# Optimization experiments

Measured on AMD Instinct MI355X. Metric: run time of the kernel, lower is better.

The kernel has to match this reference:

```python
import jax, jax.numpy as jnp
import numpy as np
import math

EMB = 2048
NH = 16
HD = EMB // NH
T = 4096
EPS = 1e-5


def setup_inputs() -> dict:
    key = jax.random.key(0)
    ks = jax.random.split(key, 8)
    lim = 1.0 / math.sqrt(EMB)
    q = jax.random.normal(ks[0], (T, EMB), dtype=jnp.float32)
    k = jax.random.normal(ks[1], (T, EMB), dtype=jnp.float32)
    v = jax.random.normal(ks[2], (T, EMB), dtype=jnp.float32)
    Wq = jax.random.uniform(ks[3], (EMB, EMB), minval=-lim, maxval=lim, dtype=jnp.float32)
    Wk = jax.random.uniform(ks[4], (EMB, EMB), minval=-lim, maxval=lim, dtype=jnp.float32)
    Wv = jax.random.uniform(ks[5], (EMB, EMB), minval=-lim, maxval=lim, dtype=jnp.float32)
    Wo = jax.random.uniform(ks[6], (EMB, EMB), minval=-lim, maxval=lim, dtype=jnp.float32)
    ln_w = jnp.ones((EMB,), dtype=jnp.float32)
    mask = jnp.tril(jnp.ones((T, T), dtype=jnp.int32))  # causal
    return {"q": q, "k": k, "v": v, "Wq": Wq, "Wk": Wk, "Wv": Wv,
            "Wo": Wo, "ln_w": ln_w, "mask": mask}


def reference(q, k, v, Wq, Wk, Wv, Wo, ln_w, mask):
    scale = 1.0 / math.sqrt(HD)
    # projections (Linear is weight @ x, i.e. x @ W^T)
    Q = (q @ Wq.T).reshape(T, NH, HD).transpose(1, 0, 2)   # [nh, T, hd]
    K = (k @ Wk.T).reshape(T, NH, HD).transpose(1, 0, 2)
    V = (v @ Wv.T).reshape(T, NH, HD).transpose(1, 0, 2)
    A = jnp.einsum('htd,hsd->hts', Q, K) * scale           # [nh, T, T]
    A = jnp.where(mask != 0, A, -jnp.inf)
    P = jax.nn.softmax(A, axis=-1)
    y = jnp.einsum('hts,hsd->htd', P, V)                   # [nh, T, hd]
    y = y.transpose(1, 0, 2).reshape(T, EMB)               # concat heads
    y = y @ Wo.T
    # deterministic dropout = identity; add residue; per-token LayerNorm (scale only)
    x = y + q
    mu = jnp.mean(x, axis=-1, keepdims=True)
    var = jnp.var(x, axis=-1, keepdims=True)
    return (x - mu) * jax.lax.rsqrt(var + EPS) * ln_w
```

## Files before the change

### kernel.cpp

```cpp
#include <hip/hip_runtime.h>

typedef __bf16 bf16x8 __attribute__((ext_vector_type(8)));
typedef __bf16 bf16x2_t __attribute__((ext_vector_type(2)));
typedef float f32x4 __attribute__((ext_vector_type(4)));
typedef float f32x16 __attribute__((ext_vector_type(16)));
typedef unsigned int u32x4 __attribute__((ext_vector_type(4)));
typedef unsigned short u16x8 __attribute__((ext_vector_type(8)));

#define EMB 2048
#define NH 16
#define HD 128
#define TSEQ 4096

__device__ __forceinline__ unsigned short f2bf(float x) {
  unsigned int u = __builtin_bit_cast(unsigned int, x);
  u += 0x7fffu + ((u >> 16) & 1u);
  return (unsigned short)(u >> 16);
}

__device__ __forceinline__ float bf2f(unsigned short u) {
  unsigned int x = ((unsigned int)u) << 16;
  return __builtin_bit_cast(float, x);
}

__device__ __forceinline__ float ex2(float x) { return __builtin_amdgcn_exp2f(x); }

__device__ __forceinline__ void gl_lds16(const void* g, void* l) {
  __builtin_amdgcn_global_load_lds((__attribute__((address_space(1))) void*)(void*)g,
                                   (__attribute__((address_space(3))) void*)l, 16, 0, 0);
}

template <typename OutT>
__device__ __forceinline__ void store_out(OutT* p, float v) {
  if constexpr (sizeof(OutT) == 2) { *p = f2bf(v); } else { *p = v; }
}

__global__ __launch_bounds__(256) void cvt_all(const float* __restrict__ q, const float* __restrict__ k,
                                               const float* __restrict__ v, const float* __restrict__ Wq,
                                               const float* __restrict__ Wk, const float* __restrict__ Wv,
                                               const float* __restrict__ Wo,
                                               unsigned short* qb, unsigned short* kb, unsigned short* vb,
                                               unsigned short* Wqb, unsigned short* Wkb, unsigned short* Wvb,
                                               unsigned short* Wob) {
  const int SX = TSEQ * EMB / 8;
  const int SW = EMB * EMB / 8;
  int i = blockIdx.x * 256 + threadIdx.x;
  const float* src; unsigned short* dst; int off;
  if (i < 3 * SX) {
    int seg = i >> 20; off = i & (SX - 1);
    src = (seg == 0) ? q : (seg == 1) ? k : v;
    dst = (seg == 0) ? qb : (seg == 1) ? kb : vb;
  } else {
    int j = i - 3 * SX;
    int seg = j >> 19; off = j & (SW - 1);
    src = (seg == 0) ? Wq : (seg == 1) ? Wk : (seg == 2) ? Wv : Wo;
    dst = (seg == 0) ? Wqb : (seg == 1) ? Wkb : (seg == 2) ? Wvb : Wob;
  }
  const float4* p = (const float4*)src + (size_t)off * 2;
  float4 a = p[0], b = p[1];
  u32x4 r;
  r.x = (unsigned)f2bf(a.x) | ((unsigned)f2bf(a.y) << 16);
  r.y = (unsigned)f2bf(a.z) | ((unsigned)f2bf(a.w) << 16);
  r.z = (unsigned)f2bf(b.x) | ((unsigned)f2bf(b.y) << 16);
  r.w = (unsigned)f2bf(b.z) | ((unsigned)f2bf(b.w) << 16);
  ((u32x4*)dst)[off] = r;
}

template <typename OutT>
__device__ __forceinline__ void gemm_body(const unsigned short* __restrict__ A,
                                          const unsigned short* __restrict__ B,
                                          OutT* __restrict__ C,
                                          int m0, int n0, int N, int K, char* smem, float oscale) {
  const int t = threadIdx.x;
  const int l = t & 63, lg = l >> 4, l15 = l & 15;
  const int w = t >> 6, wm = w >> 1, wn = w & 1;

  f32x4 acc[4][4] = {};

  const int rowS = t >> 2;
  const int cbS = (t & 3) * 16;
  const int swS = cbS ^ ((rowS & 3) << 4);
  const char* Ab = (const char*)A + ((size_t)(m0 + rowS) * K) * 2;
  const char* Bb = (const char*)B + ((size_t)(n0 + rowS) * K) * 2;
  const size_t rowStep = (size_t)64 * K * 2;

  auto stage = [&](int buf, int kt) {
    const int ktB = kt * 2;
    char* sA = smem + buf * 8192;
    char* sB = smem + 16384 + buf * 8192;
    gl_lds16(Ab + ktB + swS, sA + t * 16);
    gl_lds16(Ab + rowStep + ktB + swS, sA + 4096 + t * 16);
    gl_lds16(Bb + ktB + swS, sB + t * 16);
    gl_lds16(Bb + rowStep + ktB + swS, sB + 4096 + t * 16);
  };

  const int nIter = K / 32;
  stage(0, 0);
  int cur = 0;
  for (int it = 0; it < nIter; ++it) {
    if (it + 1 < nIter) {
      stage(cur ^ 1, (it + 1) * 32);
      asm volatile("s_waitcnt vmcnt(4)" ::: "memory");
    } else {
      asm volatile("s_waitcnt vmcnt(0)" ::: "memory");
    }
    __builtin_amdgcn_s_barrier();

    const char* sA = smem + cur * 8192;
    const char* sB = smem + 16384 + cur * 8192;
    const int rsw = (l15 & 3) << 4;
    bf16x8 af[4], bfr[4];
#pragma unroll
    for (int m = 0; m < 4; m++) {
      const int r = wm * 64 + m * 16 + l15;
      af[m] = *(const bf16x8*)(sA + r * 64 + ((lg * 16) ^ rsw));
    }
#pragma unroll
    for (int n = 0; n < 4; n++) {
      const int r = wn * 64 + n * 16 + l15;
      bfr[n] = *(const bf16x8*)(sB + r * 64 + ((lg * 16) ^ rsw));
    }
#pragma unroll
    for (int m = 0; m < 4; m++)
#pragma unroll
      for (int n = 0; n < 4; n++)
        acc[m][n] = __builtin_amdgcn_mfma_f32_16x16x32_bf16(af[m], bfr[n], acc[m][n], 0, 0, 0);

    __builtin_amdgcn_s_barrier();
    cur ^= 1;
  }

#pragma unroll
  for (int m = 0; m < 4; m++) {
    int row = m0 + wm * 64 + m * 16 + 4 * lg;
#pragma unroll
    for (int n = 0; n < 4; n++) {
      int col = n0 + wn * 64 + n * 16 + l15;
#pragma unroll
      for (int i = 0; i < 4; i++)
        store_out(C + (size_t)(row + i) * N + col, acc[m][n][i] * oscale);
    }
  }
}

__global__ __launch_bounds__(256) void gemm_qkv(const unsigned short* __restrict__ qb,
                                                const unsigned short* __restrict__ kb,
                                                const unsigned short* __restrict__ vb,
                                                const unsigned short* __restrict__ Wq,
                                                const unsigned short* __restrict__ Wk,
                                                const unsigned short* __restrict__ Wv,
                                                unsigned short* Qo, unsigned short* Ko, unsigned short* Vto) {
  __shared__ char smem[32768];
  const int bx = blockIdx.x;
  const int z = bx >> 9, r = bx & 511;
  const unsigned short* A; const unsigned short* B; unsigned short* C;
  int N, m0, n0; float sc;
  if (z == 0)      { A = qb; B = Wq; C = Qo;  N = EMB;  n0 = (r & 15) << 7; m0 = (r >> 4) << 7; sc = 0.12751743f; }
  else if (z == 1) { A = kb; B = Wk; C = Ko;  N = EMB;  n0 = (r & 15) << 7; m0 = (r >> 4) << 7; sc = 1.0f; }
  else             { A = Wv; B = vb; C = Vto; N = TSEQ; n0 = (r & 31) << 7; m0 = (r >> 5) << 7; sc = 1.0f; }
  gemm_body<unsigned short>(A, B, C, m0, n0, N, EMB, smem, sc);
}

__global__ __launch_bounds__(256) void gemm_o(const unsigned short* __restrict__ A,
                                              const unsigned short* __restrict__ B,
                                              float* __restrict__ C) {
  __shared__ char smem[32768];
  gemm_body<float>(A, B, C, blockIdx.y * 128, blockIdx.x * 128, EMB, EMB, smem, 1.0f);
}

__global__ __launch_bounds__(256, 2) void attn_kernel(const unsigned short* __restrict__ Q,
                                                      const unsigned short* __restrict__ Kp,
                                                      const unsigned short* __restrict__ Vt,
                                                      unsigned short* __restrict__ slots,
                                                      float* __restrict__ lbuf) {
  __shared__ char sK[2][16384];
  __shared__ char sV[3][16384];
  const int t = threadIdx.x, l = t & 63, w = t >> 6;
  const int l31 = l & 31, hh = l >> 5;
  const int b = blockIdx.x;
  const int h = b >> 5;
  const int p = (b >> 1) & 15;
  const int half = b & 1;
  const int slotBase = (h * 16 + p) * 3;

  const int q0A = 128 * p, q0B = 128 * (31 - p);
  const int swi = (half == 0) ? (2 * p + 2) : 64;
  const int kvOff = 31 - 2 * p;

  int q0 = (half == 0) ? q0A : q0B;
  int qrow = q0 + w * 32 + l31;

  auto kvof = [&](int gi) -> int {
    if (half == 0) return (gi < swi) ? gi * 64 : (gi - swi) * 64;
    return (kvOff + gi) * 64;
  };

  bf16x8 qf[8];
#pragma unroll
  for (int kd = 0; kd < 8; kd++)
    qf[kd] = *(const bf16x8*)(Q + (size_t)qrow * EMB + h * HD + kd * 16 + hh * 8);

  f32x16 o[4] = {};
  float l_run = 0.0f;

  const int rK = t >> 4, cK = (t & 15) * 16;
  const int rV = t >> 3, cV = (t & 7) * 16;
  const char* Kb = (const char*)Kp;
  const char* Vb = (const char*)Vt;

  auto stage = [&](int kbuf, int vbuf, int kv0) {
#pragma unroll
    for (int c = 0; c < 4; c++) {
      int rowK = c * 16 + rK;
      gl_lds16(Kb + (size_t)(kv0 + rowK) * (EMB * 2) + h * (HD * 2) + (cK ^ ((rowK & 15) << 4)),
               sK[kbuf] + c * 4096 + t * 16);
      int rowV = c * 32 + rV;
      gl_lds16(Vb + (size_t)(h * HD + rowV) * (TSEQ * 2) + kv0 * 2 + (cV ^ ((rowV & 7) << 4)),
               sV[vbuf] + c * 4096 + t * 16);
    }
  };

  auto writeout = [&](int slotId) {
    unsigned short* S = slots + (size_t)slotId * (128 * 128);
    const int r = w * 32 + l31;
    float lt = l_run + __shfl_xor(l_run, 32, 64);
    if (hh == 0) lbuf[slotId * 128 + r] = lt;
#pragma unroll
    for (int hdm = 0; hdm < 4; hdm++)
#pragma unroll
      for (int rq = 0; rq < 4; rq++) {
        ushort4 st;
        st.x = f2bf(o[hdm][4 * rq + 0]);
        st.y = f2bf(o[hdm][4 * rq + 1]);
        st.z = f2bf(o[hdm][4 * rq + 2]);
        st.w = f2bf(o[hdm][4 * rq + 3]);
        *(ushort4*)(S + r * 128 + hdm * 32 + 8 * rq + 4 * hh) = st;
      }
  };

  stage(0, 0, kvof(0));
  int kc = 0, vc = 0, vn = 1;
  for (int gi = 0; gi < 33; ++gi) {
    if (half == 0 && gi == swi) {
      writeout(slotBase + 0);
#pragma unroll
      for (int hdm = 0; hdm < 4; hdm++)
#pragma unroll
        for (int i = 0; i < 16; i++) o[hdm][i] = 0.0f;
      l_run = 0.0f;
      q0 = q0B;
      qrow = q0 + w * 32 + l31;
#pragma unroll
      for (int kd = 0; kd < 8; kd++)
        qf[kd] = *(const bf16x8*)(Q + (size_t)qrow * EMB + h * HD + kd * 16 + hh * 8);
    }
    const int kv0 = kvof(gi);
    if (gi + 1 < 33) {
      stage(kc ^ 1, vn, kvof(gi + 1));
      asm volatile("s_waitcnt vmcnt(8)" ::: "memory");
    } else {
      asm volatile("s_waitcnt vmcnt(0)" ::: "memory");
    }
    __builtin_amdgcn_s_barrier();

    const char* KB = sK[kc];
    const char* VB = sV[vc];

    f32x16 s[2];
#pragma unroll
    for (int i = 0; i < 16; i++) { s[0][i] = -8.0f; s[1][i] = -8.0f; }
    __builtin_amdgcn_s_setprio(1);
#pragma unroll
    for (int kvm = 0; kvm < 2; kvm++) {
      const int rowA = kvm * 32 + l31;
      const int swz = (rowA & 15) << 4;
#pragma unroll
      for (int kd = 0; kd < 8; kd++) {
        bf16x8 kf = *(const bf16x8*)(KB + rowA * 256 + ((kd * 32 + hh * 16) ^ swz));
        s[kvm] = __builtin_amdgcn_mfma_f32_32x32x16_bf16(kf, qf[kd], s[kvm], 0, 0, 0);
      }
    }
    __builtin_amdgcn_s_setprio(0);
    __builtin_amdgcn_s_barrier();

    const bool diag = (kv0 + 64 > q0);
    if (diag) {
#pragma unroll
      for (int kvm = 0; kvm < 2; kvm++)
#pragma unroll
        for (int i = 0; i < 16; i++)
          if (kv0 + kvm * 32 + (i & 3) + 8 * (i >> 2) + 4 * hh > qrow) s[kvm][i] = -1e30f;
    }
    float psum = 0.0f;
    unsigned int wb[16];
#pragma unroll
    for (int kvm = 0; kvm < 2; kvm++)
#pragma unroll
      for (int m = 0; m < 8; m++) {
        float p0 = ex2(s[kvm][2 * m + 0]);
        float p1 = ex2(s[kvm][2 * m + 1]);
        psum += p0 + p1;
        bf16x2_t pk; pk[0] = (__bf16)p0; pk[1] = (__bf16)p1;
        wb[kvm * 8 + m] = __builtin_bit_cast(unsigned int, pk);
      }
    l_run += psum;

    __builtin_amdgcn_s_setprio(1);
#pragma unroll
    for (int kvm = 0; kvm < 2; kvm++)
#pragma unroll
      for (int sx = 0; sx < 2; sx++) {
        const int base = kvm * 8 + 4 * sx;
        const unsigned int a0 = wb[base + 0], a1 = wb[base + 1];
        const unsigned int b0 = wb[base + 2], b1 = wb[base + 3];
        const unsigned int snd0 = hh ? a0 : b0;
        const unsigned int snd1 = hh ? a1 : b1;
        const unsigned int rcv0 = (unsigned int)__shfl_xor((int)snd0, 32, 64);
        const unsigned int rcv1 = (unsigned int)__shfl_xor((int)snd1, 32, 64);
        u32x4 pw;
        pw.x = hh ? rcv0 : a0;
        pw.y = hh ? rcv1 : a1;
        pw.z = hh ? b0 : rcv0;
        pw.w = hh ? b1 : rcv1;
        const bf16x8 pfrag = __builtin_bit_cast(bf16x8, pw);
        const int ks = kvm * 2 + sx;
#pragma unroll
        for (int hdm = 0; hdm < 4; hdm++) {
          const int rowA = hdm * 32 + l31;
          bf16x8 vf = *(const bf16x8*)(VB + rowA * 128 + ((ks * 32 + hh * 16) ^ ((rowA & 7) << 4)));
          o[hdm] = __builtin_amdgcn_mfma_f32_32x32x16_bf16(vf, pfrag, o[hdm], 0, 0, 0);
        }
      }
    __builtin_amdgcn_s_setprio(0);

    kc ^= 1;
    vc = vn;
    vn = (vn == 2) ? 0 : vn + 1;
  }

  writeout(slotBase + ((half == 0) ? 1 : 2));
}

__global__ __launch_bounds__(256) void merge_kernel(const unsigned short* __restrict__ slots,
                                                    const float* __restrict__ lbuf,
                                                    unsigned short* __restrict__ Y) {
  const int tile = blockIdx.x;
  const int h = tile >> 5, tt = tile & 31;
  const int p = (tt <= 15) ? tt : 31 - tt;
  const int base = (h * 16 + p) * 3;
  const int t = threadIdx.x;
  const int r = t >> 1;
  const int c0 = (t & 1) * 64;
  unsigned short* yp = Y + (size_t)(128 * tt + r) * EMB + h * HD + c0;
  if (tt <= 15) {
    const unsigned short* S = slots + (size_t)(base + 0) * (128 * 128) + r * 128 + c0;
    const float inv = 1.0f / lbuf[(base + 0) * 128 + r];
#pragma unroll
    for (int j = 0; j < 8; j++) {
      u16x8 a = ((const u16x8*)S)[j];
      u16x8 ov;
#pragma unroll
      for (int e = 0; e < 8; e++) ov[e] = f2bf(bf2f(a[e]) * inv);
      ((u16x8*)yp)[j] = ov;
    }
  } else {
    const unsigned short* S0 = slots + (size_t)(base + 1) * (128 * 128) + r * 128 + c0;
    const unsigned short* S1 = slots + (size_t)(base + 2) * (128 * 128) + r * 128 + c0;
    const float inv = 1.0f / (lbuf[(base + 1) * 128 + r] + lbuf[(base + 2) * 128 + r]);
#pragma unroll
    for (int j = 0; j < 8; j++) {
      u16x8 a = ((const u16x8*)S0)[j];
      u16x8 c = ((const u16x8*)S1)[j];
      u16x8 ov;
#pragma unroll
      for (int e = 0; e < 8; e++) ov[e] = f2bf((bf2f(a[e]) + bf2f(c[e])) * inv);
      ((u16x8*)yp)[j] = ov;
    }
  }
}

__global__ __launch_bounds__(256) void ln_kernel(const float* __restrict__ y2,
                                                 const float* __restrict__ qin,
                                                 const float* __restrict__ lnw,
                                                 float* __restrict__ out) {
  const int row = blockIdx.x, t = threadIdx.x;
  const float4* Y = (const float4*)(y2 + (size_t)row * EMB);
  const float4* Qv = (const float4*)(qin + (size_t)row * EMB);
  float4 a = Y[t], b = Qv[t];
  float4 x0, x1;
  x0.x = a.x + b.x; x0.y = a.y + b.y; x0.z = a.z + b.z; x0.w = a.w + b.w;
  a = Y[t + 256]; b = Qv[t + 256];
  x1.x = a.x + b.x; x1.y = a.y + b.y; x1.z = a.z + b.z; x1.w = a.w + b.w;
  float s = x0.x + x0.y + x0.z + x0.w + x1.x + x1.y + x1.z + x1.w;
  float s2 = x0.x * x0.x + x0.y * x0.y + x0.z * x0.z + x0.w * x0.w +
             x1.x * x1.x + x1.y * x1.y + x1.z * x1.z + x1.w * x1.w;
#pragma unroll
  for (int d = 1; d < 64; d <<= 1) {
    s += __shfl_xor(s, d, 64);
    s2 += __shfl_xor(s2, d, 64);
  }
  __shared__ float red[8];
  if ((t & 63) == 0) { red[(t >> 6) * 2] = s; red[(t >> 6) * 2 + 1] = s2; }
  __syncthreads();
  s = red[0] + red[2] + red[4] + red[6];
  s2 = red[1] + red[3] + red[5] + red[7];
  float mu = s * (1.0f / EMB);
  float var = s2 * (1.0f / EMB) - mu * mu;
  float r = rsqrtf(var + 1e-5f);
  float4 w0 = ((const float4*)lnw)[t], w1 = ((const float4*)lnw)[t + 256];
  float4 o0, o1;
  o0.x = (x0.x - mu) * r * w0.x; o0.y = (x0.y - mu) * r * w0.y;
  o0.z = (x0.z - mu) * r * w0.z; o0.w = (x0.w - mu) * r * w0.w;
  o1.x = (x1.x - mu) * r * w1.x; o1.y = (x1.y - mu) * r * w1.y;
  o1.z = (x1.z - mu) * r * w1.z; o1.w = (x1.w - mu) * r * w1.w;
  ((float4*)(out + (size_t)row * EMB))[t] = o0;
  ((float4*)(out + (size_t)row * EMB))[t + 256] = o1;
}

extern "C" void kernel_launch(void* const* d_in, const int* in_sizes, int n_in,
                              void* d_out, int out_size, void* d_ws, size_t ws_size,
                              hipStream_t stream) {
  const float* q = (const float*)d_in[0];
  const float* k = (const float*)d_in[1];
  const float* v = (const float*)d_in[2];
  const float* Wq = (const float*)d_in[3];
  const float* Wk = (const float*)d_in[4];
  const float* Wv = (const float*)d_in[5];
  const float* Wo = (const float*)d_in[6];
  const float* lnw = (const float*)d_in[7];
  float* out = (float*)d_out;
  char* ws = (char*)d_ws;

  const size_t WB = (size_t)EMB * EMB * 2;
  const size_t XB = (size_t)TSEQ * EMB * 2;
  unsigned short* Wq_b = (unsigned short*)(ws + 0 * WB);
  unsigned short* Wk_b = (unsigned short*)(ws + 1 * WB);
  unsigned short* Wv_b = (unsigned short*)(ws + 2 * WB);
  unsigned short* Wo_b = (unsigned short*)(ws + 3 * WB);
  unsigned short* qb   = (unsigned short*)(ws + 4 * WB);
  unsigned short* kb   = (unsigned short*)(ws + 4 * WB + XB);
  unsigned short* vb   = (unsigned short*)(ws + 4 * WB + 2 * XB);
  unsigned short* Qb   = (unsigned short*)(ws + 4 * WB + 3 * XB);
  unsigned short* Kb   = (unsigned short*)(ws + 4 * WB + 4 * XB);
  unsigned short* Vtb  = (unsigned short*)(ws + 4 * WB + 5 * XB);
  unsigned short* yb   = qb;
  unsigned short* slots = (unsigned short*)(ws + 4 * WB + XB);
  float* lbuf = (float*)(ws + 4 * WB + XB + (size_t)768 * 128 * 128 * 2);
  float* y2 = (float*)(ws + 4 * WB + XB);

  cvt_all<<<20480, 256, 0, stream>>>(q, k, v, Wq, Wk, Wv, Wo,
                                     qb, kb, vb, Wq_b, Wk_b, Wv_b, Wo_b);

  gemm_qkv<<<1536, 256, 0, stream>>>(qb, kb, vb, Wq_b, Wk_b, Wv_b, Qb, Kb, Vtb);

  attn_kernel<<<512, 256, 0, stream>>>(Qb, Kb, Vtb, slots, lbuf);

  merge_kernel<<<512, 256, 0, stream>>>(slots, lbuf, yb);

  gemm_o<<<dim3(16, 32), 256, 0, stream>>>(yb, Wo_b, y2);

  ln_kernel<<<TSEQ, 256, 0, stream>>>(y2, q, lnw, out);
}
```

Measured before the change: 325.4 us.

## Use 32x32x16 MFMA in GEMMs and remap workgroups XCD-contiguously

The shared GEMM body moves from 16x16x32 MFMA tiles to 32x32x16 tiles, which halves the number of MFMA issues and LDS fragment loads per wave per k-step. The epilogue is rewritten for the 32x32 accumulator layout. Both GEMM kernels also remap block IDs so that consecutive tiles land on the same XCD (bx&7 striding), aiming for better L2 reuse. The output store pattern changes and may coalesce differently.

```diff
diff --git a/kernel.cpp b/kernel.cpp
--- a/kernel.cpp
+++ b/kernel.cpp
@@ -72,10 +72,11 @@
                                           OutT* __restrict__ C,
                                           int m0, int n0, int N, int K, char* smem, float oscale) {
   const int t = threadIdx.x;
-  const int l = t & 63, lg = l >> 4, l15 = l & 15;
+  const int l = t & 63;
+  const int l31 = l & 31, hh = l >> 5;
   const int w = t >> 6, wm = w >> 1, wn = w & 1;
 
-  f32x4 acc[4][4] = {};
+  f32x16 acc[2][2] = {};
 
   const int rowS = t >> 2;
   const int cbS = (t & 3) * 16;
@@ -108,39 +109,47 @@
 
     const char* sA = smem + cur * 8192;
     const char* sB = smem + 16384 + cur * 8192;
-    const int rsw = (l15 & 3) << 4;
-    bf16x8 af[4], bfr[4];
-#pragma unroll
-    for (int m = 0; m < 4; m++) {
-      const int r = wm * 64 + m * 16 + l15;
-      af[m] = *(const bf16x8*)(sA + r * 64 + ((lg * 16) ^ rsw));
-    }
-#pragma unroll
-    for (int n = 0; n < 4; n++) {
-      const int r = wn * 64 + n * 16 + l15;
-      bfr[n] = *(const bf16x8*)(sB + r * 64 + ((lg * 16) ^ rsw));
-    }
-#pragma unroll
-    for (int m = 0; m < 4; m++)
-#pragma unroll
-      for (int n = 0; n < 4; n++)
-        acc[m][n] = __builtin_amdgcn_mfma_f32_16x16x32_bf16(af[m], bfr[n], acc[m][n], 0, 0, 0);
+    bf16x8 af[2][2], bfr[2][2];
+#pragma unroll
+    for (int fm = 0; fm < 2; fm++) {
+      const int r = wm * 64 + fm * 32 + l31;
+      const int sw = (r & 3) << 4;
+#pragma unroll
+      for (int ks = 0; ks < 2; ks++)
+        af[fm][ks] = *(const bf16x8*)(sA + r * 64 + ((ks * 32 + hh * 16) ^ sw));
+    }
+#pragma unroll
+    for (int fn = 0; fn < 2; fn++) {
+      const int r = wn * 64 + fn * 32 + l31;
+      const int sw = (r & 3) << 4;
+#pragma unroll
+      for (int ks = 0; ks < 2; ks++)
+        bfr[fn][ks] = *(const bf16x8*)(sB + r * 64 + ((ks * 32 + hh * 16) ^ sw));
+    }
+#pragma unroll
+    for (int ks = 0; ks < 2; ks++)
+#pragma unroll
+      for (int fm = 0; fm < 2; fm++)
+#pragma unroll
+        for (int fn = 0; fn < 2; fn++)
+          acc[fm][fn] = __builtin_amdgcn_mfma_f32_32x32x16_bf16(af[fm][ks], bfr[fn][ks],
+                                                                acc[fm][fn], 0, 0, 0);
 
     __builtin_amdgcn_s_barrier();
     cur ^= 1;
   }
 
 #pragma unroll
-  for (int m = 0; m < 4; m++) {
-    int row = m0 + wm * 64 + m * 16 + 4 * lg;
-#pragma unroll
-    for (int n = 0; n < 4; n++) {
-      int col = n0 + wn * 64 + n * 16 + l15;
-#pragma unroll
-      for (int i = 0; i < 4; i++)
-        store_out(C + (size_t)(row + i) * N + col, acc[m][n][i] * oscale);
-    }
-  }
+  for (int fm = 0; fm < 2; fm++)
+#pragma unroll
+    for (int fn = 0; fn < 2; fn++) {
+      const int col = n0 + wn * 64 + fn * 32 + l31;
+#pragma unroll
+      for (int reg = 0; reg < 16; reg++) {
+        const int row = m0 + wm * 64 + fm * 32 + (reg & 3) + 8 * (reg >> 2) + 4 * hh;
+        store_out(C + (size_t)row * N + col, acc[fm][fn][reg] * oscale);
+      }
+    }
 }
 
 __global__ __launch_bounds__(256) void gemm_qkv(const unsigned short* __restrict__ qb,
@@ -152,7 +161,8 @@
                                                 unsigned short* Qo, unsigned short* Ko, unsigned short* Vto) {
   __shared__ char smem[32768];
   const int bx = blockIdx.x;
-  const int z = bx >> 9, r = bx & 511;
+  const int wg = (bx & 7) * 192 + (bx >> 3);
+  const int z = wg >> 9, r = wg & 511;
   const unsigned short* A; const unsigned short* B; unsigned short* C;
   int N, m0, n0; float sc;
   if (z == 0)      { A = qb; B = Wq; C = Qo;  N = EMB;  n0 = (r & 15) << 7; m0 = (r >> 4) << 7; sc = 0.12751743f; }
@@ -165,7 +175,9 @@
                                               const unsigned short* __restrict__ B,
                                               float* __restrict__ C) {
   __shared__ char smem[32768];
-  gemm_body<float>(A, B, C, blockIdx.y * 128, blockIdx.x * 128, EMB, EMB, smem, 1.0f);
+  const int bx = blockIdx.x;
+  const int wg = (bx & 7) * 64 + (bx >> 3);
+  gemm_body<float>(A, B, C, (wg >> 4) * 128, (wg & 15) * 128, EMB, EMB, smem, 1.0f);
 }
 
 __global__ __launch_bounds__(256, 2) void attn_kernel(const unsigned short* __restrict__ Q,
@@ -457,7 +469,7 @@
 
   merge_kernel<<<512, 256, 0, stream>>>(slots, lbuf, yb);
 
-  gemm_o<<<dim3(16, 32), 256, 0, stream>>>(yb, Wo_b, y2);
+  gemm_o<<<512, 256, 0, stream>>>(yb, Wo_b, y2);
 
   ln_kernel<<<TSEQ, 256, 0, stream>>>(y2, q, lnw, out);
 }
```

Result: slower. 333.0 us (+2.4%).
